# Kernel tuning notes

Measured on AMD Instinct MI355X. Metric: run time of the kernel, lower is better.

## Reference

```python
import jax, jax.numpy as jnp
import numpy as np

B, L, D = 4, 4096, 1024  # batch, seq_len, d_model


def setup_inputs() -> dict:
    key = jax.random.key(0)
    k0, k1, k2 = jax.random.split(key, 3)
    x = jax.random.normal(k0, (B, L, D), dtype=jnp.float32)
    # Dense(d_model*3) applied to x: kernel [D, 3D], bias [3D]
    W_proj = jax.random.normal(k1, (D, 3 * D), dtype=jnp.float32) / np.sqrt(D)
    b_proj = jnp.zeros((3 * D,), dtype=jnp.float32)
    # Output Dense(d_model): kernel [D, D], bias [D]
    W_out = jax.random.normal(k2, (D, D), dtype=jnp.float32) / np.sqrt(D)
    b_out = jnp.zeros((D,), dtype=jnp.float32)
    return {"x": x, "W_proj": W_proj, "b_proj": b_proj,
            "W_out": W_out, "b_out": b_out,
            "layer_idx": 0, "num_layers": 12}


def reference(x, W_proj, b_proj, W_out, b_out, layer_idx, num_layers):
    # x: [B, L, D] -> x_proj: [B, L, 3D]
    x_proj = jnp.einsum('bld,de->ble', x, W_proj) + b_proj
    gate_input, forget_input, output_gate = jnp.split(x_proj, 3, axis=-1)
    # NOTE: in the source, forget_gate / input_gate / k / v / the lax.scan
    # recurrence are defined but never used to produce the output (dead code).
    # The live path is exactly:
    out = gate_input * jax.nn.sigmoid(output_gate)          # [B, L, D]
    out = jnp.einsum('bld,de->ble', out, W_out) + b_out     # [B, L, D]
    # Dropout is deterministic (training=False) -> identity.
    return out
```

## Files before the change

kernel.cpp:

```cpp
#include <hip/hip_runtime.h>
#include <hip/hip_bf16.h>


#define MTOT 16384
#define DM   1024
#define MEG  (1024 * 1024)

typedef __bf16 bf16x8 __attribute__((ext_vector_type(8)));
typedef float  f32x4  __attribute__((ext_vector_type(4)));

#define AS1 __attribute__((address_space(1)))
#define AS3 __attribute__((address_space(3)))

static __device__ __forceinline__ void async_load16(const void* g, void* l) {
    __builtin_amdgcn_global_load_lds((const AS1 void*)g, (AS3 void*)l, 16, 0, 0);
}

static __device__ __forceinline__ unsigned short f2bf(float f) {
    __hip_bfloat16 h = __float2bfloat16(f);
    return *(unsigned short*)&h;
}

__global__ __launch_bounds__(256)
void conv_x(const float* __restrict__ x, unsigned short* __restrict__ dst) {
    const size_t i = ((size_t)blockIdx.x * 256 + threadIdx.x) * 8;
    const f32x4 a = *(const f32x4*)(x + i);
    const f32x4 b = *(const f32x4*)(x + i + 4);
    __align__(16) unsigned short o[8];
    o[0] = f2bf(a[0]); o[1] = f2bf(a[1]); o[2] = f2bf(a[2]); o[3] = f2bf(a[3]);
    o[4] = f2bf(b[0]); o[5] = f2bf(b[1]); o[6] = f2bf(b[2]); o[7] = f2bf(b[3]);
    *(uint4*)(dst + i) = *(const uint4*)o;
}

__global__ void transpose_w(const float* __restrict__ Wproj, const float* __restrict__ Wout,
                            unsigned short* __restrict__ dst0) {
    __shared__ unsigned short t[32][33];
    const int z = blockIdx.z;
    const float* src;
    unsigned short* dst;
    int ld, coff;
    if (z == 0)      { src = Wproj; ld = 3072; coff = 0;    dst = dst0; }
    else if (z == 1) { src = Wproj; ld = 3072; coff = 2048; dst = dst0 + MEG; }
    else             { src = Wout;  ld = 1024; coff = 0;    dst = dst0 + 2 * MEG; }
    const int k0 = blockIdx.x * 32;
    const int n0 = blockIdx.y * 32;
    const int tx = threadIdx.x, ty = threadIdx.y;
    for (int i = ty; i < 32; i += 8)
        t[i][tx] = f2bf(src[(size_t)(k0 + i) * ld + coff + n0 + tx]);
    __syncthreads();
    for (int i = ty; i < 32; i += 8)
        dst[(size_t)(n0 + i) * DM + k0 + tx] = t[tx][i];
}

__global__ __launch_bounds__(512)
void gemm1_fused(const unsigned short* __restrict__ X,
                 const unsigned short* __restrict__ WgT,
                 const unsigned short* __restrict__ WoT,
                 const float* __restrict__ bproj,
                 unsigned short* __restrict__ Hlo,
                 unsigned short* __restrict__ Hhi) {
    __shared__ __align__(16) unsigned short sA[2][256 * 64];
    __shared__ __align__(16) unsigned short sB[2][256 * 64];

    const int tid  = threadIdx.x;
    const int wave = tid >> 6;
    const int lane = tid & 63;
    const int wm = wave & 1;
    const int wn = wave >> 1;

    const int bid = blockIdx.x;
    const int swz = (bid & 7) * 64 + (bid >> 3);
    const int m0 = (swz >> 3) * 256;
    const int n0 = (swz & 7) * 128;

    unsigned short* __restrict__ H =
        (m0 < 8192) ? Hlo : (Hhi - (size_t)8192 * DM);

    const int rA = lane & 15;
    const int qq = lane >> 4;
    const int r7 = rA & 7;
    const int swq   = ((qq ^ (r7 & 3)) << 4);
    const int k0off = ((rA >> 2) & 1) << 6;
    const int k1off = k0off ^ 64;
    const int ldsA_base = (wm * 64 + rA) * 128 + swq;
    const int ldsB_base = (wn * 16 + rA) * 128 + swq;

    const int trow = tid >> 3;
    const int tsw  = (((tid & 7) ^ (trow & 7)) << 4);
    const char* srcA  = (const char*)X   + (size_t)(m0 + trow) * 2048 + tsw;
    const char* srcBg = (const char*)WgT + (size_t)(n0 + trow) * 2048 + tsw;
    const char* srcBo = (const char*)WoT + (size_t)(n0 + trow) * 2048 + tsw;
    char* dA = (char*)&sA[0][0] + tid * 16;
    char* dB = (char*)&sB[0][0] + tid * 16;

#define STA1(b, kt, r)  async_load16(srcA  + (kt) * 128 + (r) * 131072, dA + (b) * 32768 + (r) * 8192)
#define STBG1(b, kt, r) async_load16(srcBg + (kt) * 128 + (r) * 131072, dB + (b) * 32768 + (r) * 8192)
#define STBO1(b, kt, r) async_load16(srcBo + (kt) * 128 + (r) * 131072, dB + (b) * 32768 + (2 + (r)) * 8192)
#define LDA1(dst, bb, h, il, kof) dst = *(const bf16x8*)((const char*)sA + (bb) * 32768 + ldsA_base + (h) * 16384 + (il) * 2048 + (kof))
#define LDB1(dst, bb, mat, j, kof) dst = *(const bf16x8*)((const char*)sB + (bb) * 32768 + ldsB_base + (mat) * 16384 + (j) * 8192 + (kof))

    f32x4 aG[2][4][2], aO[2][4][2];
    bf16x8 fa[4][2], fbg[2], fbo[2];

    STA1(0, 0, 0); STA1(0, 0, 1); STA1(0, 0, 2); STA1(0, 0, 3);
    STBG1(0, 0, 0); STBG1(0, 0, 1); STBO1(0, 0, 0); STBO1(0, 0, 1);
    STBG1(1, 1, 0); STBO1(1, 1, 0); STA1(1, 1, 2); STA1(1, 1, 3);

#pragma unroll
    for (int h = 0; h < 2; ++h)
#pragma unroll
        for (int il = 0; il < 4; ++il)
#pragma unroll
            for (int jl = 0; jl < 2; ++jl) {
                aG[h][il][jl] = (f32x4){0.f, 0.f, 0.f, 0.f};
                aO[h][il][jl] = (f32x4){0.f, 0.f, 0.f, 0.f};
            }

    asm volatile("s_waitcnt vmcnt(4)" ::: "memory");
    __builtin_amdgcn_s_barrier();

#define MM1(H_, JL) do { \
    _Pragma("unroll") \
    for (int il = 0; il < 4; ++il) { \
        aG[H_][il][JL] = __builtin_amdgcn_mfma_f32_16x16x32_bf16(fa[il][0], fbg[0], aG[H_][il][JL], 0, 0, 0); \
        aO[H_][il][JL] = __builtin_amdgcn_mfma_f32_16x16x32_bf16(fa[il][0], fbo[0], aO[H_][il][JL], 0, 0, 0); \
        aG[H_][il][JL] = __builtin_amdgcn_mfma_f32_16x16x32_bf16(fa[il][1], fbg[1], aG[H_][il][JL], 0, 0, 0); \
        aO[H_][il][JL] = __builtin_amdgcn_mfma_f32_16x16x32_bf16(fa[il][1], fbo[1], aO[H_][il][JL], 0, 0, 0); \
    } } while (0)

#define PHASE_SYNC() \
    __builtin_amdgcn_s_barrier(); \
    asm volatile("s_waitcnt lgkmcnt(0)" ::: "memory"); \
    __builtin_amdgcn_sched_barrier(0)

#define TILE1(kt, b, nb) do { \
     \
    _Pragma("unroll") \
    for (int il = 0; il < 4; ++il) { LDA1(fa[il][0], b, 0, il, k0off); LDA1(fa[il][1], b, 0, il, k1off); } \
    LDB1(fbg[0], b, 0, 0, k0off); LDB1(fbg[1], b, 0, 0, k1off); \
    LDB1(fbo[0], b, 1, 0, k0off); LDB1(fbo[1], b, 1, 0, k1off); \
    if ((kt) < 15) { STA1(nb, (kt) + 1, 0); STBG1(nb, (kt) + 1, 1); } \
    PHASE_SYNC(); \
    __builtin_amdgcn_s_setprio(1); MM1(0, 0); __builtin_amdgcn_s_setprio(0); \
    __builtin_amdgcn_s_barrier(); \
     \
    _Pragma("unroll") \
    for (int il = 0; il < 4; ++il) { LDA1(fa[il][0], b, 1, il, k0off); LDA1(fa[il][1], b, 1, il, k1off); } \
    if ((kt) < 15) { STA1(nb, (kt) + 1, 1); STBO1(nb, (kt) + 1, 1); } \
    PHASE_SYNC(); \
    __builtin_amdgcn_s_setprio(1); MM1(1, 0); __builtin_amdgcn_s_setprio(0); \
    __builtin_amdgcn_s_barrier(); \
     \
    LDB1(fbg[0], b, 0, 1, k0off); LDB1(fbg[1], b, 0, 1, k1off); \
    LDB1(fbo[0], b, 1, 1, k0off); LDB1(fbo[1], b, 1, 1, k1off); \
    if ((kt) < 14) { STBG1(b, (kt) + 2, 0); STBO1(b, (kt) + 2, 0); } \
    PHASE_SYNC(); \
    __builtin_amdgcn_s_setprio(1); MM1(1, 1); __builtin_amdgcn_s_setprio(0); \
    __builtin_amdgcn_s_barrier(); \
     \
    _Pragma("unroll") \
    for (int il = 0; il < 4; ++il) { LDA1(fa[il][0], b, 0, il, k0off); LDA1(fa[il][1], b, 0, il, k1off); } \
    if ((kt) < 14) { STA1(b, (kt) + 2, 2); STA1(b, (kt) + 2, 3); } \
    PHASE_SYNC(); \
    __builtin_amdgcn_s_setprio(1); MM1(0, 1); __builtin_amdgcn_s_setprio(0); \
    if ((kt) < 14) { asm volatile("s_waitcnt vmcnt(4)" ::: "memory"); } \
    else           { asm volatile("s_waitcnt vmcnt(0)" ::: "memory"); } \
    __builtin_amdgcn_s_barrier(); \
} while (0)

#pragma unroll 1
    for (int kt2 = 0; kt2 < 16; kt2 += 2) {
        TILE1(kt2, 0, 1);
        TILE1(kt2 + 1, 1, 0);
    }
#undef TILE1
#undef MM1
#undef STA1
#undef STBG1
#undef STBO1
#undef LDA1
#undef LDB1

    const int colL = lane & 15;
    const int rowQ = (lane >> 4) * 4;
#pragma unroll
    for (int jl = 0; jl < 2; ++jl) {
        const int n = n0 + wn * 16 + jl * 64 + colL;
        const float bgv = bproj[n];
        const float bov = bproj[2048 + n];
#pragma unroll
        for (int h = 0; h < 2; ++h)
#pragma unroll
            for (int il = 0; il < 4; ++il) {
                const int mbase = m0 + wm * 64 + h * 128 + il * 16 + rowQ;
#pragma unroll
                for (int r = 0; r < 4; ++r) {
                    const float g = aG[h][il][jl][r] + bgv;
                    const float o = aO[h][il][jl][r] + bov;
                    const float hv = g * (1.0f / (1.0f + __expf(-o)));
                    H[(size_t)(mbase + r) * DM + n] = f2bf(hv);
                }
            }
    }
}

__global__ __launch_bounds__(512)
void gemm2(const unsigned short* __restrict__ Hlo,
           const unsigned short* __restrict__ Hhi,
           const unsigned short* __restrict__ Bt,
           const float* __restrict__ bout,
           float* __restrict__ Out,
           int row_base) {
    __shared__ __align__(16) unsigned short sA[2][256 * 64];
    __shared__ __align__(16) unsigned short sB[2][256 * 64];

    const int tid  = threadIdx.x;
    const int wave = tid >> 6;
    const int lane = tid & 63;
    const int wm = wave & 1;
    const int wn = wave >> 1;

    const int bid = blockIdx.x;
    const int q8  = (int)gridDim.x >> 3;
    const int swz = (bid & 7) * q8 + (bid >> 3);
    const int m0 = row_base + (swz >> 2) * 256;
    const int n0 = (swz & 3) * 256;

    const unsigned short* __restrict__ A =
        (m0 < 8192) ? (Hlo + (size_t)m0 * DM) : (Hhi + (size_t)(m0 - 8192) * DM);

    const int rA = lane & 15;
    const int qq = lane >> 4;
    const int r7 = rA & 7;
    const int swq   = ((qq ^ (r7 & 3)) << 4);
    const int k0off = ((rA >> 2) & 1) << 6;
    const int k1off = k0off ^ 64;
    const int ldsA_base = (wm * 64 + rA) * 128 + swq;
    const int ldsB_base = (wn * 16 + rA) * 128 + swq;

    const int trow = tid >> 3;
    const int tsw  = (((tid & 7) ^ (trow & 7)) << 4);
    const char* srcA = (const char*)A  + (size_t)trow * 2048 + tsw;
    const char* srcB = (const char*)Bt + (size_t)(n0 + trow) * 2048 + tsw;
    char* dA = (char*)&sA[0][0] + tid * 16;
    char* dB = (char*)&sB[0][0] + tid * 16;

#define STA2(b, kt, r) async_load16(srcA + (kt) * 128 + (r) * 131072, dA + (b) * 32768 + (r) * 8192)
#define STB2(b, kt, r) async_load16(srcB + (kt) * 128 + (r) * 131072, dB + (b) * 32768 + (r) * 8192)
#define LDA2(dst, bb, h, il, kof) dst = *(const bf16x8*)((const char*)sA + (bb) * 32768 + ldsA_base + (h) * 16384 + (il) * 2048 + (kof))
#define LDB2(dst, bb, j, kof)     dst = *(const bf16x8*)((const char*)sB + (bb) * 32768 + ldsB_base + (j) * 8192 + (kof))

    f32x4 acc[2][4][4];
    bf16x8 fa[4][2], fb[2][2];

    STA2(0, 0, 0); STA2(0, 0, 1); STA2(0, 0, 2); STA2(0, 0, 3);
    STB2(0, 0, 0); STB2(0, 0, 1); STB2(0, 0, 2); STB2(0, 0, 3);
    STB2(1, 1, 0); STB2(1, 1, 1); STA2(1, 1, 2); STA2(1, 1, 3);

#pragma unroll
    for (int h = 0; h < 2; ++h)
#pragma unroll
        for (int il = 0; il < 4; ++il)
#pragma unroll
            for (int j = 0; j < 4; ++j)
                acc[h][il][j] = (f32x4){0.f, 0.f, 0.f, 0.f};

    asm volatile("s_waitcnt vmcnt(4)" ::: "memory");
    __builtin_amdgcn_s_barrier();

#define MM2(H_, JB) do { \
    _Pragma("unroll") \
    for (int il = 0; il < 4; ++il) { \
        acc[H_][il][JB]     = __builtin_amdgcn_mfma_f32_16x16x32_bf16(fa[il][0], fb[0][0], acc[H_][il][JB], 0, 0, 0); \
        acc[H_][il][JB + 1] = __builtin_amdgcn_mfma_f32_16x16x32_bf16(fa[il][0], fb[1][0], acc[H_][il][JB + 1], 0, 0, 0); \
        acc[H_][il][JB]     = __builtin_amdgcn_mfma_f32_16x16x32_bf16(fa[il][1], fb[0][1], acc[H_][il][JB], 0, 0, 0); \
        acc[H_][il][JB + 1] = __builtin_amdgcn_mfma_f32_16x16x32_bf16(fa[il][1], fb[1][1], acc[H_][il][JB + 1], 0, 0, 0); \
    } } while (0)

#define PHASE_SYNC2() \
    __builtin_amdgcn_s_barrier(); \
    asm volatile("s_waitcnt lgkmcnt(0)" ::: "memory"); \
    __builtin_amdgcn_sched_barrier(0)

#define TILE2(kt, b, nb) do { \
     \
    _Pragma("unroll") \
    for (int il = 0; il < 4; ++il) { LDA2(fa[il][0], b, 0, il, k0off); LDA2(fa[il][1], b, 0, il, k1off); } \
    LDB2(fb[0][0], b, 0, k0off); LDB2(fb[0][1], b, 0, k1off); \
    LDB2(fb[1][0], b, 1, k0off); LDB2(fb[1][1], b, 1, k1off); \
    if ((kt) < 15) { STA2(nb, (kt) + 1, 0); STB2(nb, (kt) + 1, 2); } \
    PHASE_SYNC2(); \
    __builtin_amdgcn_s_setprio(1); MM2(0, 0); __builtin_amdgcn_s_setprio(0); \
    __builtin_amdgcn_s_barrier(); \
     \
    _Pragma("unroll") \
    for (int il = 0; il < 4; ++il) { LDA2(fa[il][0], b, 1, il, k0off); LDA2(fa[il][1], b, 1, il, k1off); } \
    if ((kt) < 15) { STA2(nb, (kt) + 1, 1); STB2(nb, (kt) + 1, 3); } \
    PHASE_SYNC2(); \
    __builtin_amdgcn_s_setprio(1); MM2(1, 0); __builtin_amdgcn_s_setprio(0); \
    __builtin_amdgcn_s_barrier(); \
     \
    LDB2(fb[0][0], b, 2, k0off); LDB2(fb[0][1], b, 2, k1off); \
    LDB2(fb[1][0], b, 3, k0off); LDB2(fb[1][1], b, 3, k1off); \
    if ((kt) < 14) { STB2(b, (kt) + 2, 0); STB2(b, (kt) + 2, 1); } \
    PHASE_SYNC2(); \
    __builtin_amdgcn_s_setprio(1); MM2(1, 2); __builtin_amdgcn_s_setprio(0); \
    __builtin_amdgcn_s_barrier(); \
     \
    _Pragma("unroll") \
    for (int il = 0; il < 4; ++il) { LDA2(fa[il][0], b, 0, il, k0off); LDA2(fa[il][1], b, 0, il, k1off); } \
    if ((kt) < 14) { STA2(b, (kt) + 2, 2); STA2(b, (kt) + 2, 3); } \
    PHASE_SYNC2(); \
    __builtin_amdgcn_s_setprio(1); MM2(0, 2); __builtin_amdgcn_s_setprio(0); \
    if ((kt) < 14) { asm volatile("s_waitcnt vmcnt(4)" ::: "memory"); } \
    else           { asm volatile("s_waitcnt vmcnt(0)" ::: "memory"); } \
    __builtin_amdgcn_s_barrier(); \
} while (0)

#pragma unroll 1
    for (int kt2 = 0; kt2 < 16; kt2 += 2) {
        TILE2(kt2, 0, 1);
        TILE2(kt2 + 1, 1, 0);
    }
#undef TILE2
#undef MM2
#undef STA2
#undef STB2
#undef LDA2
#undef LDB2

    const int colL = lane & 15;
    const int rowQ = (lane >> 4) * 4;
#pragma unroll
    for (int j = 0; j < 4; ++j) {
        const int n = n0 + wn * 16 + j * 64 + colL;
        const float bv = bout[n];
#pragma unroll
        for (int h = 0; h < 2; ++h)
#pragma unroll
            for (int il = 0; il < 4; ++il) {
                const int mbase = m0 + wm * 64 + h * 128 + il * 16 + rowQ;
#pragma unroll
                for (int r = 0; r < 4; ++r)
                    Out[(size_t)(mbase + r) * DM + n] = acc[h][il][j][r] + bv;
            }
    }
}

extern "C" void kernel_launch(void* const* d_in, const int* in_sizes, int n_in,
                              void* d_out, int out_size, void* d_ws, size_t ws_size,
                              hipStream_t stream) {
    const float* x     = (const float*)d_in[0];
    const float* Wproj = (const float*)d_in[1];
    const float* bproj = (const float*)d_in[2];
    const float* Wout  = (const float*)d_in[3];
    const float* bout  = (const float*)d_in[4];
    float* out = (float*)d_out;

    unsigned short* Xb  = (unsigned short*)d_out;
    unsigned short* WgT   = (unsigned short*)d_ws;
    unsigned short* WoT   = WgT + MEG;
    unsigned short* WoutT = WgT + 2 * MEG;
    unsigned short* Hws   = WgT + 3 * MEG;

    const bool big_ws = ws_size >= (size_t)19 * MEG * 2;

    unsigned short* Hlo = big_ws ? Hws : ((unsigned short*)d_out + 16 * MEG);
    unsigned short* Hhi = big_ws ? (Hws + (size_t)8192 * DM) : Hws;

    conv_x<<<(MTOT * DM) / (256 * 8), 256, 0, stream>>>(x, Xb);

    transpose_w<<<dim3(32, 32, 3), dim3(32, 8, 1), 0, stream>>>(Wproj, Wout, WgT);

    gemm1_fused<<<512, 512, 0, stream>>>(Xb, WgT, WoT, bproj, Hlo, Hhi);

    if (big_ws) {
        gemm2<<<256, 512, 0, stream>>>(Hlo, Hhi, WoutT, bout, out, 0);
    } else {
        gemm2<<<128, 512, 0, stream>>>(Hlo, Hhi, WoutT, bout, out, 0);
        gemm2<<<128, 512, 0, stream>>>(Hlo, Hhi, WoutT, bout, out, 8192);
    }
}
```

Before: 244.1 us.

## Restructure GEMM pipelines: two-phase k-tiles and 256x128 tiles for output GEMM

The gated first GEMM now loads both B column groups at once and runs two MFMA phases per k-tile instead of four. That drops the extra barriers per phase at the cost of more fragment registers. The output GEMM switches from 256x256 to 256x128 block tiles with a 4x2 wave layout, halving the B shared-memory buffer and doubling the grid to 512 blocks. Together these aim to cut synchronisation overhead and improve CU occupancy and balance. The trade-off is lower per-block data reuse in the second GEMM.

```diff
diff --git a/kernel.cpp b/kernel.cpp
--- a/kernel.cpp
+++ b/kernel.cpp
@@ -100,11 +100,11 @@
 #define LDB1(dst, bb, mat, j, kof) dst = *(const bf16x8*)((const char*)sB + (bb) * 32768 + ldsB_base + (mat) * 16384 + (j) * 8192 + (kof))
 
     f32x4 aG[2][4][2], aO[2][4][2];
-    bf16x8 fa[4][2], fbg[2], fbo[2];
+    bf16x8 fa[4][2], fbg[2][2], fbo[2][2];
 
     STA1(0, 0, 0); STA1(0, 0, 1); STA1(0, 0, 2); STA1(0, 0, 3);
     STBG1(0, 0, 0); STBG1(0, 0, 1); STBO1(0, 0, 0); STBO1(0, 0, 1);
-    STBG1(1, 1, 0); STBO1(1, 1, 0); STA1(1, 1, 2); STA1(1, 1, 3);
+    STA1(1, 1, 0); STA1(1, 1, 1); STBG1(1, 1, 0); STBO1(1, 1, 0);
 
 #pragma unroll
     for (int h = 0; h < 2; ++h)
@@ -119,50 +119,37 @@
     asm volatile("s_waitcnt vmcnt(4)" ::: "memory");
     __builtin_amdgcn_s_barrier();
 
-#define MM1(H_, JL) do { \
+#define MM1(H_) do { \
     _Pragma("unroll") \
     for (int il = 0; il < 4; ++il) { \
-        aG[H_][il][JL] = __builtin_amdgcn_mfma_f32_16x16x32_bf16(fa[il][0], fbg[0], aG[H_][il][JL], 0, 0, 0); \
-        aO[H_][il][JL] = __builtin_amdgcn_mfma_f32_16x16x32_bf16(fa[il][0], fbo[0], aO[H_][il][JL], 0, 0, 0); \
-        aG[H_][il][JL] = __builtin_amdgcn_mfma_f32_16x16x32_bf16(fa[il][1], fbg[1], aG[H_][il][JL], 0, 0, 0); \
-        aO[H_][il][JL] = __builtin_amdgcn_mfma_f32_16x16x32_bf16(fa[il][1], fbo[1], aO[H_][il][JL], 0, 0, 0); \
-    } } while (0)
-
-#define PHASE_SYNC() \
-    __builtin_amdgcn_s_barrier(); \
-    asm volatile("s_waitcnt lgkmcnt(0)" ::: "memory"); \
-    __builtin_amdgcn_sched_barrier(0)
+        _Pragma("unroll") \
+        for (int jl = 0; jl < 2; ++jl) { \
+            aG[H_][il][jl] = __builtin_amdgcn_mfma_f32_16x16x32_bf16(fa[il][0], fbg[jl][0], aG[H_][il][jl], 0, 0, 0); \
+            aO[H_][il][jl] = __builtin_amdgcn_mfma_f32_16x16x32_bf16(fa[il][0], fbo[jl][0], aO[H_][il][jl], 0, 0, 0); \
+            aG[H_][il][jl] = __builtin_amdgcn_mfma_f32_16x16x32_bf16(fa[il][1], fbg[jl][1], aG[H_][il][jl], 0, 0, 0); \
+            aO[H_][il][jl] = __builtin_amdgcn_mfma_f32_16x16x32_bf16(fa[il][1], fbo[jl][1], aO[H_][il][jl], 0, 0, 0); \
+        } } } while (0)
 
 #define TILE1(kt, b, nb) do { \
      \
     _Pragma("unroll") \
     for (int il = 0; il < 4; ++il) { LDA1(fa[il][0], b, 0, il, k0off); LDA1(fa[il][1], b, 0, il, k1off); } \
-    LDB1(fbg[0], b, 0, 0, k0off); LDB1(fbg[1], b, 0, 0, k1off); \
-    LDB1(fbo[0], b, 1, 0, k0off); LDB1(fbo[1], b, 1, 0, k1off); \
-    if ((kt) < 15) { STA1(nb, (kt) + 1, 0); STBG1(nb, (kt) + 1, 1); } \
-    PHASE_SYNC(); \
-    __builtin_amdgcn_s_setprio(1); MM1(0, 0); __builtin_amdgcn_s_setprio(0); \
+    _Pragma("unroll") \
+    for (int jl = 0; jl < 2; ++jl) { \
+        LDB1(fbg[jl][0], b, 0, jl, k0off); LDB1(fbg[jl][1], b, 0, jl, k1off); \
+        LDB1(fbo[jl][0], b, 1, jl, k0off); LDB1(fbo[jl][1], b, 1, jl, k1off); } \
+    if ((kt) < 15) { STA1(nb, (kt) + 1, 2); STA1(nb, (kt) + 1, 3); STBG1(nb, (kt) + 1, 1); STBO1(nb, (kt) + 1, 1); } \
+    asm volatile("s_waitcnt lgkmcnt(0)" ::: "memory"); \
+    __builtin_amdgcn_sched_barrier(0); \
+    __builtin_amdgcn_s_setprio(1); MM1(0); __builtin_amdgcn_s_setprio(0); \
     __builtin_amdgcn_s_barrier(); \
      \
     _Pragma("unroll") \
     for (int il = 0; il < 4; ++il) { LDA1(fa[il][0], b, 1, il, k0off); LDA1(fa[il][1], b, 1, il, k1off); } \
-    if ((kt) < 15) { STA1(nb, (kt) + 1, 1); STBO1(nb, (kt) + 1, 1); } \
-    PHASE_SYNC(); \
-    __builtin_amdgcn_s_setprio(1); MM1(1, 0); __builtin_amdgcn_s_setprio(0); \
-    __builtin_amdgcn_s_barrier(); \
-     \
-    LDB1(fbg[0], b, 0, 1, k0off); LDB1(fbg[1], b, 0, 1, k1off); \
-    LDB1(fbo[0], b, 1, 1, k0off); LDB1(fbo[1], b, 1, 1, k1off); \
-    if ((kt) < 14) { STBG1(b, (kt) + 2, 0); STBO1(b, (kt) + 2, 0); } \
-    PHASE_SYNC(); \
-    __builtin_amdgcn_s_setprio(1); MM1(1, 1); __builtin_amdgcn_s_setprio(0); \
-    __builtin_amdgcn_s_barrier(); \
-     \
-    _Pragma("unroll") \
-    for (int il = 0; il < 4; ++il) { LDA1(fa[il][0], b, 0, il, k0off); LDA1(fa[il][1], b, 0, il, k1off); } \
-    if ((kt) < 14) { STA1(b, (kt) + 2, 2); STA1(b, (kt) + 2, 3); } \
-    PHASE_SYNC(); \
-    __builtin_amdgcn_s_setprio(1); MM1(0, 1); __builtin_amdgcn_s_setprio(0); \
+    if ((kt) < 14) { STA1(b, (kt) + 2, 0); STA1(b, (kt) + 2, 1); STBG1(b, (kt) + 2, 0); STBO1(b, (kt) + 2, 0); } \
+    asm volatile("s_waitcnt lgkmcnt(0)" ::: "memory"); \
+    __builtin_amdgcn_sched_barrier(0); \
+    __builtin_amdgcn_s_setprio(1); MM1(1); __builtin_amdgcn_s_setprio(0); \
     if ((kt) < 14) { asm volatile("s_waitcnt vmcnt(4)" ::: "memory"); } \
     else           { asm volatile("s_waitcnt vmcnt(0)" ::: "memory"); } \
     __builtin_amdgcn_s_barrier(); \
@@ -212,19 +199,19 @@
            float* __restrict__ Out,
            int row_base) {
     __shared__ __align__(16) unsigned short sA[2][256 * 64];
-    __shared__ __align__(16) unsigned short sB[2][256 * 64];
+    __shared__ __align__(16) unsigned short sB[2][128 * 64];
 
     const int tid  = threadIdx.x;
     const int wave = tid >> 6;
     const int lane = tid & 63;
-    const int wm = wave & 1;
-    const int wn = wave >> 1;
+    const int wm = wave & 3;
+    const int wn = wave >> 2;
 
     const int bid = blockIdx.x;
     const int q8  = (int)gridDim.x >> 3;
     const int swz = (bid & 7) * q8 + (bid >> 3);
-    const int m0 = row_base + (swz >> 2) * 256;
-    const int n0 = (swz & 3) * 256;
+    const int m0 = row_base + (swz >> 3) * 256;
+    const int n0 = (swz & 7) * 128;
 
     const unsigned short* __restrict__ A =
         (m0 < 8192) ? (Hlo + (size_t)m0 * DM) : (Hhi + (size_t)(m0 - 8192) * DM);
@@ -236,7 +223,7 @@
     const int k0off = ((rA >> 2) & 1) << 6;
     const int k1off = k0off ^ 64;
     const int ldsA_base = (wm * 64 + rA) * 128 + swq;
-    const int ldsB_base = (wn * 16 + rA) * 128 + swq;
+    const int ldsB_base = (wn * 64 + rA) * 128 + swq;
 
     const int trow = tid >> 3;
     const int tsw  = (((tid & 7) ^ (trow & 7)) << 4);
@@ -246,73 +233,49 @@
     char* dB = (char*)&sB[0][0] + tid * 16;
 
 #define STA2(b, kt, r) async_load16(srcA + (kt) * 128 + (r) * 131072, dA + (b) * 32768 + (r) * 8192)
-#define STB2(b, kt, r) async_load16(srcB + (kt) * 128 + (r) * 131072, dB + (b) * 32768 + (r) * 8192)
-#define LDA2(dst, bb, h, il, kof) dst = *(const bf16x8*)((const char*)sA + (bb) * 32768 + ldsA_base + (h) * 16384 + (il) * 2048 + (kof))
-#define LDB2(dst, bb, j, kof)     dst = *(const bf16x8*)((const char*)sB + (bb) * 32768 + ldsB_base + (j) * 8192 + (kof))
-
-    f32x4 acc[2][4][4];
-    bf16x8 fa[4][2], fb[2][2];
+#define STB2(b, kt, r) async_load16(srcB + (kt) * 128 + (r) * 131072, dB + (b) * 16384 + (r) * 8192)
+#define LDA2(dst, bb, il, kof) dst = *(const bf16x8*)((const char*)sA + (bb) * 32768 + ldsA_base + (il) * 2048 + (kof))
+#define LDB2(dst, bb, jl, kof) dst = *(const bf16x8*)((const char*)sB + (bb) * 16384 + ldsB_base + (jl) * 2048 + (kof))
+
+    f32x4 acc[4][4];
+    bf16x8 fa[4][2], fb[4][2];
 
     STA2(0, 0, 0); STA2(0, 0, 1); STA2(0, 0, 2); STA2(0, 0, 3);
-    STB2(0, 0, 0); STB2(0, 0, 1); STB2(0, 0, 2); STB2(0, 0, 3);
-    STB2(1, 1, 0); STB2(1, 1, 1); STA2(1, 1, 2); STA2(1, 1, 3);
-
-#pragma unroll
-    for (int h = 0; h < 2; ++h)
-#pragma unroll
-        for (int il = 0; il < 4; ++il)
-#pragma unroll
-            for (int j = 0; j < 4; ++j)
-                acc[h][il][j] = (f32x4){0.f, 0.f, 0.f, 0.f};
-
-    asm volatile("s_waitcnt vmcnt(4)" ::: "memory");
+    STB2(0, 0, 0); STB2(0, 0, 1);
+    STA2(1, 1, 0); STA2(1, 1, 1); STB2(1, 1, 0);
+
+#pragma unroll
+    for (int il = 0; il < 4; ++il)
+#pragma unroll
+        for (int j = 0; j < 4; ++j) acc[il][j] = (f32x4){0.f, 0.f, 0.f, 0.f};
+
+    asm volatile("s_waitcnt vmcnt(3)" ::: "memory");
     __builtin_amdgcn_s_barrier();
 
-#define MM2(H_, JB) do { \
+#define MM2(JB) do { \
     _Pragma("unroll") \
     for (int il = 0; il < 4; ++il) { \
-        acc[H_][il][JB]     = __builtin_amdgcn_mfma_f32_16x16x32_bf16(fa[il][0], fb[0][0], acc[H_][il][JB], 0, 0, 0); \
-        acc[H_][il][JB + 1] = __builtin_amdgcn_mfma_f32_16x16x32_bf16(fa[il][0], fb[1][0], acc[H_][il][JB + 1], 0, 0, 0); \
-        acc[H_][il][JB]     = __builtin_amdgcn_mfma_f32_16x16x32_bf16(fa[il][1], fb[0][1], acc[H_][il][JB], 0, 0, 0); \
-        acc[H_][il][JB + 1] = __builtin_amdgcn_mfma_f32_16x16x32_bf16(fa[il][1], fb[1][1], acc[H_][il][JB + 1], 0, 0, 0); \
+        acc[il][JB]     = __builtin_amdgcn_mfma_f32_16x16x32_bf16(fa[il][0], fb[JB][0], acc[il][JB], 0, 0, 0); \
+        acc[il][JB + 1] = __builtin_amdgcn_mfma_f32_16x16x32_bf16(fa[il][0], fb[JB + 1][0], acc[il][JB + 1], 0, 0, 0); \
+        acc[il][JB]     = __builtin_amdgcn_mfma_f32_16x16x32_bf16(fa[il][1], fb[JB][1], acc[il][JB], 0, 0, 0); \
+        acc[il][JB + 1] = __builtin_amdgcn_mfma_f32_16x16x32_bf16(fa[il][1], fb[JB + 1][1], acc[il][JB + 1], 0, 0, 0); \
     } } while (0)
-
-#define PHASE_SYNC2() \
-    __builtin_amdgcn_s_barrier(); \
-    asm volatile("s_waitcnt lgkmcnt(0)" ::: "memory"); \
-    __builtin_amdgcn_sched_barrier(0)
 
 #define TILE2(kt, b, nb) do { \
      \
     _Pragma("unroll") \
-    for (int il = 0; il < 4; ++il) { LDA2(fa[il][0], b, 0, il, k0off); LDA2(fa[il][1], b, 0, il, k1off); } \
-    LDB2(fb[0][0], b, 0, k0off); LDB2(fb[0][1], b, 0, k1off); \
-    LDB2(fb[1][0], b, 1, k0off); LDB2(fb[1][1], b, 1, k1off); \
-    if ((kt) < 15) { STA2(nb, (kt) + 1, 0); STB2(nb, (kt) + 1, 2); } \
-    PHASE_SYNC2(); \
-    __builtin_amdgcn_s_setprio(1); MM2(0, 0); __builtin_amdgcn_s_setprio(0); \
+    for (int il = 0; il < 4; ++il) { LDA2(fa[il][0], b, il, k0off); LDA2(fa[il][1], b, il, k1off); } \
+    _Pragma("unroll") \
+    for (int jl = 0; jl < 4; ++jl) { LDB2(fb[jl][0], b, jl, k0off); LDB2(fb[jl][1], b, jl, k1off); } \
+    if ((kt) < 15) { STA2(nb, (kt) + 1, 2); STA2(nb, (kt) + 1, 3); STB2(nb, (kt) + 1, 1); } \
+    asm volatile("s_waitcnt lgkmcnt(0)" ::: "memory"); \
+    __builtin_amdgcn_sched_barrier(0); \
+    __builtin_amdgcn_s_setprio(1); MM2(0); __builtin_amdgcn_s_setprio(0); \
     __builtin_amdgcn_s_barrier(); \
      \
-    _Pragma("unroll") \
-    for (int il = 0; il < 4; ++il) { LDA2(fa[il][0], b, 1, il, k0off); LDA2(fa[il][1], b, 1, il, k1off); } \
-    if ((kt) < 15) { STA2(nb, (kt) + 1, 1); STB2(nb, (kt) + 1, 3); } \
-    PHASE_SYNC2(); \
-    __builtin_amdgcn_s_setprio(1); MM2(1, 0); __builtin_amdgcn_s_setprio(0); \
-    __builtin_amdgcn_s_barrier(); \
-     \
-    LDB2(fb[0][0], b, 2, k0off); LDB2(fb[0][1], b, 2, k1off); \
-    LDB2(fb[1][0], b, 3, k0off); LDB2(fb[1][1], b, 3, k1off); \
-    if ((kt) < 14) { STB2(b, (kt) + 2, 0); STB2(b, (kt) + 2, 1); } \
-    PHASE_SYNC2(); \
-    __builtin_amdgcn_s_setprio(1); MM2(1, 2); __builtin_amdgcn_s_setprio(0); \
-    __builtin_amdgcn_s_barrier(); \
-     \
-    _Pragma("unroll") \
-    for (int il = 0; il < 4; ++il) { LDA2(fa[il][0], b, 0, il, k0off); LDA2(fa[il][1], b, 0, il, k1off); } \
-    if ((kt) < 14) { STA2(b, (kt) + 2, 2); STA2(b, (kt) + 2, 3); } \
-    PHASE_SYNC2(); \
-    __builtin_amdgcn_s_setprio(1); MM2(0, 2); __builtin_amdgcn_s_setprio(0); \
-    if ((kt) < 14) { asm volatile("s_waitcnt vmcnt(4)" ::: "memory"); } \
+    if ((kt) < 14) { STA2(b, (kt) + 2, 0); STA2(b, (kt) + 2, 1); STB2(b, (kt) + 2, 0); } \
+    __builtin_amdgcn_s_setprio(1); MM2(2); __builtin_amdgcn_s_setprio(0); \
+    if ((kt) < 14) { asm volatile("s_waitcnt vmcnt(3)" ::: "memory"); } \
     else           { asm volatile("s_waitcnt vmcnt(0)" ::: "memory"); } \
     __builtin_amdgcn_s_barrier(); \
 } while (0)
@@ -332,18 +295,16 @@
     const int colL = lane & 15;
     const int rowQ = (lane >> 4) * 4;
 #pragma unroll
-    for (int j = 0; j < 4; ++j) {
-        const int n = n0 + wn * 16 + j * 64 + colL;
+    for (int jl = 0; jl < 4; ++jl) {
+        const int n = n0 + wn * 64 + jl * 16 + colL;
         const float bv = bout[n];
 #pragma unroll
-        for (int h = 0; h < 2; ++h)
-#pragma unroll
-            for (int il = 0; il < 4; ++il) {
-                const int mbase = m0 + wm * 64 + h * 128 + il * 16 + rowQ;
-#pragma unroll
-                for (int r = 0; r < 4; ++r)
-                    Out[(size_t)(mbase + r) * DM + n] = acc[h][il][j][r] + bv;
-            }
+        for (int il = 0; il < 4; ++il) {
+            const int mbase = m0 + wm * 64 + il * 16 + rowQ;
+#pragma unroll
+            for (int r = 0; r < 4; ++r)
+                Out[(size_t)(mbase + r) * DM + n] = acc[il][jl][r] + bv;
+        }
     }
 }
 
@@ -375,9 +336,9 @@
     gemm1_fused<<<512, 512, 0, stream>>>(Xb, WgT, WoT, bproj, Hlo, Hhi);
 
     if (big_ws) {
+        gemm2<<<512, 512, 0, stream>>>(Hlo, Hhi, WoutT, bout, out, 0);
+    } else {
         gemm2<<<256, 512, 0, stream>>>(Hlo, Hhi, WoutT, bout, out, 0);
-    } else {
-        gemm2<<<128, 512, 0, stream>>>(Hlo, Hhi, WoutT, bout, out, 0);
-        gemm2<<<128, 512, 0, stream>>>(Hlo, Hhi, WoutT, bout, out, 8192);
-    }
-}
+        gemm2<<<256, 512, 0, stream>>>(Hlo, Hhi, WoutT, bout, out, 8192);
+    }
+}
```

Measured after the change: 243.9 us. No clear change (-0.1%).
